# Performance work log

Hardware: AMD Instinct MI355X
Metric: run time of the kernel (lower is better)

## Reference

```python
import jax, jax.numpy as jnp
import numpy as np

B, T, H, L = 64, 256, 1024, 5

def setup_inputs() -> dict:
    key = jax.random.key(0)
    ks = jax.random.split(key, 8)
    s = 0.02  # init scale
    inp = {
        'x': jax.random.normal(ks[0], (B, T, H), jnp.float32),
        'Wi': jax.random.normal(ks[1], (L, 2 * H, H), jnp.float32) * s,
        'bi': jnp.zeros((L, H), jnp.float32),
        'Wf': jax.random.normal(ks[2], (L, 2 * H, H), jnp.float32) * s,
        'bf': jnp.zeros((L, H), jnp.float32),
        'Wc': jax.random.normal(ks[3], (L, 2 * H, H), jnp.float32) * s,
        'bc': jnp.zeros((L, H), jnp.float32),
        'Wo': jax.random.normal(ks[4], (L, 2 * H, H), jnp.float32) * s,
        'bo': jnp.zeros((L, H), jnp.float32),
        'Wfc': jax.random.normal(ks[5], (H, 1), jnp.float32) * s,
        'bfc': jnp.zeros((1,), jnp.float32),
    }
    return inp


def _lstm_layer(x_tbh, Wi, bi, Wf, bf, Wc, bc, Wo, bo):
    # x_tbh: [T, B, H]; returns hidden sequence [T, B, H]
    Bsz = x_tbh.shape[1]
    h0 = jnp.zeros((Bsz, Wi.shape[1]), x_tbh.dtype)
    c0 = jnp.zeros_like(h0)

    def step(carry, x_t):
        h, c = carry
        u = jnp.concatenate([x_t, h], axis=-1)  # [B, 2H]
        i = jax.nn.sigmoid(u @ Wi + bi)
        f = jax.nn.sigmoid(u @ Wf + bf)
        g = jnp.tanh(u @ Wc + bc)
        c_new = c * f + i * g
        o = jax.nn.sigmoid(u @ Wo + bo)
        h_new = o * jnp.tanh(c_new)
        return (h_new, c_new), h_new

    _, hs = jax.lax.scan(step, (h0, c0), x_tbh)
    return hs


def reference(x, Wi, bi, Wf, bf, Wc, bc, Wo, bo, Wfc, bfc):
    # x: [B, T, H]. 5 stacked hand-rolled LSTM layers (dropout = eval identity),
    # then FC on the last timestep's hidden state.
    seq = jnp.transpose(x, (1, 0, 2))  # [T, B, H]
    for l in range(L):
        seq = _lstm_layer(seq, Wi[l], bi[l], Wf[l], bf[l], Wc[l], bc[l], Wo[l], bo[l])
    last = seq[-1]  # [B, H]
    return last @ Wfc + bfc  # [B, 1]
```

## Files before the change

### kernel.cpp

```cpp
#include <hip/hip_runtime.h>
#include <hip/hip_bf16.h>


using bf16x8 = __attribute__((ext_vector_type(8))) __bf16;
using f32x4  = __attribute__((ext_vector_type(4))) float;

#define Tn 256
#define Bn 64
#define Hn 1024

#define MFMA16(a, b, c) __builtin_amdgcn_mfma_f32_16x16x32_bf16((a), (b), (c), 0, 0, 0)

__global__ void convW(const float* __restrict__ Wi, const float* __restrict__ Wf,
                      const float* __restrict__ Wc, const float* __restrict__ Wo,
                      __bf16* __restrict__ Wperm) {
    int gid = blockIdx.x * 256 + threadIdx.x;
    int k8  = gid & 255;
    int col = (gid >> 8) & 31;
    int cb  = (gid >> 13) & 127;
    int l   = gid >> 20;
    int g   = col >> 3;
    int uu  = col & 7;
    int unit = cb * 8 + uu;
    const float* Wg = (g == 0) ? Wi : (g == 1) ? Wf : (g == 2) ? Wc : Wo;
    const float* src = Wg + ((size_t)l * 2048 + k8 * 8) * 1024 + unit;
    bf16x8 v;
#pragma unroll
    for (int j = 0; j < 8; ++j) v[j] = (__bf16)src[(size_t)j * 1024];
    int p   = k8 >> 7;
    int kg  = (k8 >> 5) & 3;
    int kt  = (k8 >> 2) & 7;
    int lh  = k8 & 3;
    int nf  = col >> 4;
    int l15 = col & 15;
    int frag = ((p * 4 + kg) * 8 + kt) * 2 + nf;
    int lane = lh * 16 + l15;
    size_t dst = ((size_t)l * 128 + cb) * 131072 + (size_t)frag * 1024 + lane * 16;
    *(bf16x8*)((char*)Wperm + dst) = v;
}

__global__ void convX(const float* __restrict__ x, __bf16* __restrict__ seq) {
    int gid = blockIdx.x * 256 + threadIdx.x;
    int k8 = gid & 127;
    int b  = (gid >> 7) & 63;
    int t  = gid >> 13;
    const float* src = x + ((size_t)b * Tn + t) * Hn + k8 * 8;
    bf16x8 v;
#pragma unroll
    for (int j = 0; j < 8; ++j) v[j] = (__bf16)src[j];
    *(bf16x8*)(seq + (size_t)gid * 8) = v;
}

__device__ __forceinline__ void load8_coh(const __bf16* p,
        bf16x8& a0, bf16x8& a1, bf16x8& a2, bf16x8& a3,
        bf16x8& a4, bf16x8& a5, bf16x8& a6, bf16x8& a7) {
    asm volatile(
        "global_load_dwordx4 %0, %8, off sc0 sc1\n\t"
        "global_load_dwordx4 %1, %8, off offset:64 sc0 sc1\n\t"
        "global_load_dwordx4 %2, %8, off offset:128 sc0 sc1\n\t"
        "global_load_dwordx4 %3, %8, off offset:192 sc0 sc1\n\t"
        "global_load_dwordx4 %4, %8, off offset:256 sc0 sc1\n\t"
        "global_load_dwordx4 %5, %8, off offset:320 sc0 sc1\n\t"
        "global_load_dwordx4 %6, %8, off offset:384 sc0 sc1\n\t"
        "global_load_dwordx4 %7, %8, off offset:448 sc0 sc1\n\t"
        "s_waitcnt vmcnt(0)"
        : "=&v"(a0), "=&v"(a1), "=&v"(a2), "=&v"(a3),
          "=&v"(a4), "=&v"(a5), "=&v"(a6), "=&v"(a7)
        : "v"(p) : "memory");
    __builtin_amdgcn_sched_barrier(0);
}

__device__ __forceinline__ void store_coh_u32(void* p, unsigned v) {
    asm volatile("global_store_dword %0, %1, off sc0 sc1" :: "v"(p), "v"(v) : "memory");
}

__device__ __forceinline__ unsigned load_coh_u32(const void* p) {
    unsigned v;
    asm volatile("global_load_dword %0, %1, off sc0 sc1\n\ts_waitcnt vmcnt(0)"
                 : "=v"(v) : "v"(p) : "memory");
    return v;
}

__device__ __forceinline__ float fsigmoid(float z) {
    return __builtin_amdgcn_rcpf(1.f + __builtin_amdgcn_exp2f(-1.44269504089f * z));
}
__device__ __forceinline__ float ftanh(float z) {
    return 1.f - 2.f * __builtin_amdgcn_rcpf(1.f + __builtin_amdgcn_exp2f(2.88539008178f * z));
}

__global__ __launch_bounds__(512, 2) void lstm_all(
    __bf16* __restrict__ seqA, __bf16* __restrict__ seqB,
    const __bf16* __restrict__ Wperm,
    const float* __restrict__ bip, const float* __restrict__ bfp,
    const float* __restrict__ bcp, const float* __restrict__ bop,
    unsigned* __restrict__ bar) {
    extern __shared__ char smem[];
    float* zp = (float*)(smem + 131072);

    const int tid  = threadIdx.x;
    const int bid  = blockIdx.x;
    const int rb   = bid & 1;
    const int cb   = bid >> 1;
    const int lane = tid & 63;
    const int kg   = (tid >> 6) & 3;
    const int mg   = tid >> 8;
    const int l15  = lane & 15;
    const int lhi  = lane >> 4;
    const int arow = rb * 32 + mg * 16 + l15;
    const unsigned lane16 = (unsigned)lane << 4;

    unsigned* myflag = bar + ((size_t)rb * 128 + cb) * 32;
    const unsigned* wflag = bar + ((size_t)rb * 128 + kg * 32 + (lane & 31)) * 32;

    __bf16* inp  = seqA;
    __bf16* outp = seqB;

    for (int l = 0; l < 5; ++l) {
        __builtin_amdgcn_fence(__ATOMIC_ACQUIRE, "agent");

        const char* Wl = (const char*)Wperm + ((size_t)l * 128 + cb) * 131072;
#pragma unroll
        for (int it = 0; it < 16; ++it) {
            int off = it * 8192 + tid * 16;
            *(bf16x8*)(smem + off) = *(const bf16x8*)(Wl + off);
        }
        float bia0 = 0.f, bia1 = 0.f, bia2 = 0.f, bia3 = 0.f, creg = 0.f;
        if (tid < 256) {
            int unit = cb * 8 + (tid & 7);
            bia0 = bip[l * 1024 + unit];
            bia1 = bfp[l * 1024 + unit];
            bia2 = bcp[l * 1024 + unit];
            bia3 = bop[l * 1024 + unit];
        }
        __syncthreads();

        bf16x8 bh[2][8];
#pragma unroll
        for (int nf = 0; nf < 2; ++nf)
#pragma unroll
            for (int kt = 0; kt < 8; ++kt)
                bh[nf][kt] = *(const bf16x8*)(smem +
                    ((unsigned)((((4 + kg) * 8 + kt) * 2 + nf) << 10)) + lane16);

        f32x4 acc0 = {}, acc1 = {};
        {
            const __bf16* ax = inp + (size_t)arow * Hn + kg * 256 + lhi * 8;
#pragma unroll
            for (int kt = 0; kt < 8; ++kt) {
                bf16x8 a  = *(const bf16x8*)(ax + kt * 32);
                bf16x8 b0 = *(const bf16x8*)(smem +
                    ((unsigned)(((kg * 8 + kt) * 2 + 0) << 10)) + lane16);
                bf16x8 b1 = *(const bf16x8*)(smem +
                    ((unsigned)(((kg * 8 + kt) * 2 + 1) << 10)) + lane16);
                acc0 = MFMA16(a, b0, acc0);
                acc1 = MFMA16(a, b1, acc1);
            }
        }

        for (int t = 0; t < Tn; ++t) {
            if (t > 0) {
                unsigned target = (unsigned)(l * Tn + t);
                while (true) {
                    unsigned v = load_coh_u32(wflag);
                    if (__all((int)(v >= target))) break;
                }
                bf16x8 a0, a1, a2, a3, a4, a5, a6, a7;
                load8_coh(outp + ((size_t)(t - 1) * Bn + arow) * Hn
                               + kg * 256 + lhi * 8,
                          a0, a1, a2, a3, a4, a5, a6, a7);
                acc0 = MFMA16(a0, bh[0][0], acc0); acc1 = MFMA16(a0, bh[1][0], acc1);
                acc0 = MFMA16(a1, bh[0][1], acc0); acc1 = MFMA16(a1, bh[1][1], acc1);
                acc0 = MFMA16(a2, bh[0][2], acc0); acc1 = MFMA16(a2, bh[1][2], acc1);
                acc0 = MFMA16(a3, bh[0][3], acc0); acc1 = MFMA16(a3, bh[1][3], acc1);
                acc0 = MFMA16(a4, bh[0][4], acc0); acc1 = MFMA16(a4, bh[1][4], acc1);
                acc0 = MFMA16(a5, bh[0][5], acc0); acc1 = MFMA16(a5, bh[1][5], acc1);
                acc0 = MFMA16(a6, bh[0][6], acc0); acc1 = MFMA16(a6, bh[1][6], acc1);
                acc0 = MFMA16(a7, bh[0][7], acc0); acc1 = MFMA16(a7, bh[1][7], acc1);
            }
#pragma unroll
            for (int j = 0; j < 4; ++j) {
                int row = kg * 32 + mg * 16 + 4 * lhi + j;
                zp[row * 36 + l15]      = acc0[j];
                zp[row * 36 + 16 + l15] = acc1[j];
            }
            __syncthreads();
            if (tid < 256) {
                int uu = tid & 7, eb = tid >> 3;
                float z0 = bia0, z1 = bia1, z2 = bia2, z3 = bia3;
#pragma unroll
                for (int k2 = 0; k2 < 4; ++k2) {
                    const float* zr = zp + (k2 * 32 + eb) * 36 + uu;
                    z0 += zr[0]; z1 += zr[8]; z2 += zr[16]; z3 += zr[24];
                }
                float ii = fsigmoid(z0);
                float ff = fsigmoid(z1);
                float gg = ftanh(z2);
                float oo = fsigmoid(z3);
                creg = creg * ff + ii * gg;
                float hv = oo * ftanh(creg);
                float hv2 = __shfl_xor(hv, 1);
                if (!(tid & 1)) {
                    unsigned lo = (unsigned)__builtin_bit_cast(unsigned short, (__bf16)hv);
                    unsigned hi = (unsigned)__builtin_bit_cast(unsigned short, (__bf16)hv2);
                    unsigned* dst = (unsigned*)(outp +
                        (((size_t)t * Bn + rb * 32 + eb) * Hn + cb * 8 + uu));
                    store_coh_u32(dst, lo | (hi << 16));
                }
            }
            asm volatile("s_waitcnt vmcnt(0)" ::: "memory");
            __syncthreads();
            if (tid == 0)
                store_coh_u32(myflag, (unsigned)(l * Tn + t + 1));
            acc0 = (f32x4){}; acc1 = (f32x4){};
            if (t < Tn - 1) {
                const __bf16* ax = inp + ((size_t)(t + 1) * Bn + arow) * Hn
                                       + kg * 256 + lhi * 8;
#pragma unroll
                for (int kt = 0; kt < 8; ++kt) {
                    bf16x8 a  = *(const bf16x8*)(ax + kt * 32);
                    bf16x8 b0 = *(const bf16x8*)(smem +
                        ((unsigned)(((kg * 8 + kt) * 2 + 0) << 10)) + lane16);
                    bf16x8 b1 = *(const bf16x8*)(smem +
                        ((unsigned)(((kg * 8 + kt) * 2 + 1) << 10)) + lane16);
                    acc0 = MFMA16(a, b0, acc0);
                    acc1 = MFMA16(a, b1, acc1);
                }
            }
        }
        __bf16* tmp = outp; outp = inp; inp = tmp;
    }
}

__global__ void fc_kernel(const __bf16* __restrict__ seq, const float* __restrict__ Wfc,
                          const float* __restrict__ bfc, float* __restrict__ out) {
    int b = blockIdx.x;
    int tid = threadIdx.x;
    const __bf16* h = seq + ((size_t)(Tn - 1) * Bn + b) * Hn;
    float s = 0.f;
    for (int k = tid; k < Hn; k += 256) s += (float)h[k] * Wfc[k];
#pragma unroll
    for (int off = 32; off > 0; off >>= 1) s += __shfl_down(s, off);
    __shared__ float red[4];
    if ((tid & 63) == 0) red[tid >> 6] = s;
    __syncthreads();
    if (tid == 0) out[b] = red[0] + red[1] + red[2] + red[3] + bfc[0];
}

extern "C" void kernel_launch(void* const* d_in, const int* in_sizes, int n_in,
                              void* d_out, int out_size, void* d_ws, size_t ws_size,
                              hipStream_t stream) {
    const float* x   = (const float*)d_in[0];
    const float* Wi  = (const float*)d_in[1];
    const float* bi  = (const float*)d_in[2];
    const float* Wf  = (const float*)d_in[3];
    const float* bf  = (const float*)d_in[4];
    const float* Wc  = (const float*)d_in[5];
    const float* bc  = (const float*)d_in[6];
    const float* Wo  = (const float*)d_in[7];
    const float* bo  = (const float*)d_in[8];
    const float* Wfc = (const float*)d_in[9];
    const float* bfc = (const float*)d_in[10];

    char* ws = (char*)d_ws;
    __bf16*   Wperm = (__bf16*)ws;
    __bf16*   seqA  = (__bf16*)(ws + 83886080);
    __bf16*   seqB  = (__bf16*)(ws + 83886080 + 33554432);
    unsigned* bar   = (unsigned*)(ws + 83886080 + 2 * 33554432);

    hipFuncSetAttribute((const void*)lstm_all,
                        hipFuncAttributeMaxDynamicSharedMemorySize, 149504);

    hipLaunchKernelGGL(convW, dim3(20480), dim3(256), 0, stream, Wi, Wf, Wc, Wo, Wperm);
    hipLaunchKernelGGL(convX, dim3(8192), dim3(256), 0, stream, x, seqA);
    hipMemsetAsync(bar, 0, 32768, stream);

    void* args[] = {(void*)&seqA, (void*)&seqB, (void*)&Wperm,
                    (void*)&bi, (void*)&bf, (void*)&bc, (void*)&bo, (void*)&bar};
    hipLaunchCooperativeKernel((const void*)lstm_all, dim3(256), dim3(512),
                               args, 149504, stream);

    hipLaunchKernelGGL(fc_kernel, dim3(64), dim3(256), 0, stream, seqB, Wfc, bfc,
                       (float*)d_out);
}
```

Baseline: 6.691 ms.

## Use per-wave completion flags with packed 16-byte h stores in LSTM recurrence

Each of the four gate-computing waves now publishes its own completion flag right after its hidden-state stores. This removes the block-wide barrier that used to sit before a single per-block flag. Consumers poll the flags of exactly the producer waves whose rows they need. Hidden values are packed across 8 lanes with shuffles into one 16-byte coherent store, the gate math runs at raised wave priority, and the previous-step h reads switch from coherent sc0/sc1 asm loads to plain vector loads. The plain loads risk reading stale cached data across CUs, and an extra barrier is added after the gate-sum reduction.

```diff
diff --git a/kernel.cpp b/kernel.cpp
--- a/kernel.cpp
+++ b/kernel.cpp
@@ -4,6 +4,7 @@
 
 using bf16x8 = __attribute__((ext_vector_type(8))) __bf16;
 using f32x4  = __attribute__((ext_vector_type(4))) float;
+using u32x4  = __attribute__((ext_vector_type(4))) unsigned;
 
 #define Tn 256
 #define Bn 64
@@ -51,29 +52,12 @@
     *(bf16x8*)(seq + (size_t)gid * 8) = v;
 }
 
-__device__ __forceinline__ void load8_coh(const __bf16* p,
-        bf16x8& a0, bf16x8& a1, bf16x8& a2, bf16x8& a3,
-        bf16x8& a4, bf16x8& a5, bf16x8& a6, bf16x8& a7) {
-    asm volatile(
-        "global_load_dwordx4 %0, %8, off sc0 sc1\n\t"
-        "global_load_dwordx4 %1, %8, off offset:64 sc0 sc1\n\t"
-        "global_load_dwordx4 %2, %8, off offset:128 sc0 sc1\n\t"
-        "global_load_dwordx4 %3, %8, off offset:192 sc0 sc1\n\t"
-        "global_load_dwordx4 %4, %8, off offset:256 sc0 sc1\n\t"
-        "global_load_dwordx4 %5, %8, off offset:320 sc0 sc1\n\t"
-        "global_load_dwordx4 %6, %8, off offset:384 sc0 sc1\n\t"
-        "global_load_dwordx4 %7, %8, off offset:448 sc0 sc1\n\t"
-        "s_waitcnt vmcnt(0)"
-        : "=&v"(a0), "=&v"(a1), "=&v"(a2), "=&v"(a3),
-          "=&v"(a4), "=&v"(a5), "=&v"(a6), "=&v"(a7)
-        : "v"(p) : "memory");
-    __builtin_amdgcn_sched_barrier(0);
-}
-
 __device__ __forceinline__ void store_coh_u32(void* p, unsigned v) {
     asm volatile("global_store_dword %0, %1, off sc0 sc1" :: "v"(p), "v"(v) : "memory");
 }
-
+__device__ __forceinline__ void store_coh_u32x4(void* p, u32x4 v) {
+    asm volatile("global_store_dwordx4 %0, %1, off sc0 sc1" :: "v"(p), "v"(v) : "memory");
+}
 __device__ __forceinline__ unsigned load_coh_u32(const void* p) {
     unsigned v;
     asm volatile("global_load_dword %0, %1, off sc0 sc1\n\ts_waitcnt vmcnt(0)"
@@ -109,8 +93,9 @@
     const int arow = rb * 32 + mg * 16 + l15;
     const unsigned lane16 = (unsigned)lane << 4;
 
-    unsigned* myflag = bar + ((size_t)rb * 128 + cb) * 32;
-    const unsigned* wflag = bar + ((size_t)rb * 128 + kg * 32 + (lane & 31)) * 32;
+    unsigned* myflag = bar + (rb * 4 + (tid >> 6)) * 128 + cb;
+    const unsigned* pollp = bar + (rb * 4 + 2 * mg + (lane >> 5)) * 128
+                                + kg * 32 + (lane & 31);
 
     __bf16* inp  = seqA;
     __bf16* outp = seqB;
@@ -161,13 +146,19 @@
             if (t > 0) {
                 unsigned target = (unsigned)(l * Tn + t);
                 while (true) {
-                    unsigned v = load_coh_u32(wflag);
+                    unsigned v = load_coh_u32(pollp);
                     if (__all((int)(v >= target))) break;
                 }
-                bf16x8 a0, a1, a2, a3, a4, a5, a6, a7;
-                load8_coh(outp + ((size_t)(t - 1) * Bn + arow) * Hn
-                               + kg * 256 + lhi * 8,
-                          a0, a1, a2, a3, a4, a5, a6, a7);
+                const __bf16* ah = outp + ((size_t)(t - 1) * Bn + arow) * Hn
+                                        + kg * 256 + lhi * 8;
+                bf16x8 a0 = *(const bf16x8*)(ah);
+                bf16x8 a1 = *(const bf16x8*)(ah + 32);
+                bf16x8 a2 = *(const bf16x8*)(ah + 64);
+                bf16x8 a3 = *(const bf16x8*)(ah + 96);
+                bf16x8 a4 = *(const bf16x8*)(ah + 128);
+                bf16x8 a5 = *(const bf16x8*)(ah + 160);
+                bf16x8 a6 = *(const bf16x8*)(ah + 192);
+                bf16x8 a7 = *(const bf16x8*)(ah + 224);
                 acc0 = MFMA16(a0, bh[0][0], acc0); acc1 = MFMA16(a0, bh[1][0], acc1);
                 acc0 = MFMA16(a1, bh[0][1], acc0); acc1 = MFMA16(a1, bh[1][1], acc1);
                 acc0 = MFMA16(a2, bh[0][2], acc0); acc1 = MFMA16(a2, bh[1][2], acc1);
@@ -184,33 +175,41 @@
                 zp[row * 36 + 16 + l15] = acc1[j];
             }
             __syncthreads();
+            float z0 = 0.f, z1 = 0.f, z2 = 0.f, z3 = 0.f;
             if (tid < 256) {
                 int uu = tid & 7, eb = tid >> 3;
-                float z0 = bia0, z1 = bia1, z2 = bia2, z3 = bia3;
+                z0 = bia0; z1 = bia1; z2 = bia2; z3 = bia3;
 #pragma unroll
                 for (int k2 = 0; k2 < 4; ++k2) {
                     const float* zr = zp + (k2 * 32 + eb) * 36 + uu;
                     z0 += zr[0]; z1 += zr[8]; z2 += zr[16]; z3 += zr[24];
                 }
+            }
+            __syncthreads();
+            if (tid < 256) {
+                __builtin_amdgcn_s_setprio(1);
                 float ii = fsigmoid(z0);
                 float ff = fsigmoid(z1);
                 float gg = ftanh(z2);
                 float oo = fsigmoid(z3);
                 creg = creg * ff + ii * gg;
                 float hv = oo * ftanh(creg);
-                float hv2 = __shfl_xor(hv, 1);
-                if (!(tid & 1)) {
-                    unsigned lo = (unsigned)__builtin_bit_cast(unsigned short, (__bf16)hv);
-                    unsigned hi = (unsigned)__builtin_bit_cast(unsigned short, (__bf16)hv2);
-                    unsigned* dst = (unsigned*)(outp +
-                        (((size_t)t * Bn + rb * 32 + eb) * Hn + cb * 8 + uu));
-                    store_coh_u32(dst, lo | (hi << 16));
-                }
-            }
-            asm volatile("s_waitcnt vmcnt(0)" ::: "memory");
-            __syncthreads();
-            if (tid == 0)
-                store_coh_u32(myflag, (unsigned)(l * Tn + t + 1));
+                unsigned hb = (unsigned)__builtin_bit_cast(unsigned short, (__bf16)hv);
+                unsigned d  = hb | ((unsigned)__shfl_xor((int)hb, 1) << 16);
+                unsigned d2 = (unsigned)__shfl_xor((int)d, 2);
+                unsigned e0 = (unsigned)__shfl_xor((int)d, 4);
+                unsigned e1 = (unsigned)__shfl_xor((int)d2, 4);
+                if ((lane & 7) == 0) {
+                    int eb = tid >> 3;
+                    u32x4 v4 = {d, d2, e0, e1};
+                    store_coh_u32x4(outp + (((size_t)t * Bn + rb * 32 + eb) * Hn
+                                            + cb * 8), v4);
+                }
+                asm volatile("s_waitcnt vmcnt(0)" ::: "memory");
+                if ((tid & 63) == 0)
+                    store_coh_u32(myflag, (unsigned)(l * Tn + t + 1));
+                __builtin_amdgcn_s_setprio(0);
+            }
             acc0 = (f32x4){}; acc1 = (f32x4){};
             if (t < Tn - 1) {
                 const __bf16* ax = inp + ((size_t)(t + 1) * Bn + arow) * Hn
@@ -272,7 +271,7 @@
 
     hipLaunchKernelGGL(convW, dim3(20480), dim3(256), 0, stream, Wi, Wf, Wc, Wo, Wperm);
     hipLaunchKernelGGL(convX, dim3(8192), dim3(256), 0, stream, x, seqA);
-    hipMemsetAsync(bar, 0, 32768, stream);
+    hipMemsetAsync(bar, 0, 4096, stream);
 
     void* args[] = {(void*)&seqA, (void*)&seqB, (void*)&Wperm,
                     (void*)&bi, (void*)&bf, (void*)&bc, (void*)&bo, (void*)&bar};
```

New measurement: 6.051 ms. -9.6%, faster.
